# Performance work log

Hardware: AMD Instinct MI355X
Metric: run time of the kernel (lower is better)

The kernel has to match this reference:

```python
import jax, jax.numpy as jnp
import numpy as np

H = 50  # LSTM units, fixed in the original module


def setup_inputs() -> dict:
    key = jax.random.key(0)
    ks = jax.random.split(key, 5)
    B, T, F = 4096, 365, 32
    scale = 0.1
    return {
        "x": jax.random.normal(ks[0], (B, T, F), jnp.float32),
        "kernel": jax.random.normal(ks[1], (F, 4 * H), jnp.float32) * scale,
        "rec_kernel": jax.random.normal(ks[2], (H, 4 * H), jnp.float32) * scale,
        "bias": jax.random.normal(ks[3], (4 * H,), jnp.float32) * scale,
        "dense_w": jax.random.normal(ks[4], (H, 1), jnp.float32) * scale,
        "dense_b": jnp.zeros((1,), jnp.float32),
    }


def _lstm_last_h(x, kernel, rec_kernel, bias):
    # Keras LSTM, gate order [i, f, c, o]; activation=relu, recurrent_activation=sigmoid.
    B = x.shape[0]
    # Precompute input contribution for all timesteps: [B, T, 4H]
    xg = jnp.einsum("btf,fg->btg", x, kernel) + bias
    h0 = jnp.zeros((B, H), x.dtype)
    c0 = jnp.zeros((B, H), x.dtype)

    def step(carry, xt):  # xt: [B, 4H]
        h, c = carry
        g = xt + h @ rec_kernel
        i = jax.nn.sigmoid(g[:, :H])
        f = jax.nn.sigmoid(g[:, H:2 * H])
        cand = jax.nn.relu(g[:, 2 * H:3 * H])
        o = jax.nn.sigmoid(g[:, 3 * H:])
        c_new = f * c + i * cand
        h_new = o * jax.nn.relu(c_new)
        return (h_new, c_new), None

    (h_last, _), _ = jax.lax.scan(step, (h0, c0), jnp.swapaxes(xg, 0, 1))
    return h_last  # [B, H]


def reference(x, kernel, rec_kernel, bias, dense_w, dense_b):
    h = _lstm_last_h(x, kernel, rec_kernel, bias)
    return h @ dense_w + dense_b  # [B, 1]
```

## Files before the change

kernel.cpp:

```cpp
#include <hip/hip_runtime.h>


typedef _Float16 f16;
typedef f16 f16x4 __attribute__((ext_vector_type(4)));
typedef float f32x4 __attribute__((ext_vector_type(4)));

#define T_STEPS 365
#define F_IN    32
#define H_U     50
#define NG      200
#define AST     72
#define GST     212

__global__ __launch_bounds__(256)
void lstm_fused(const float* __restrict__ x,
                const float* __restrict__ wk,
                const float* __restrict__ wr,
                const float* __restrict__ bias,
                const float* __restrict__ dw,
                const float* __restrict__ db,
                float* __restrict__ out)
{
    __shared__ f16   As[2][16 * AST];
    __shared__ float Gs[16 * GST];

    const int tid  = threadIdx.x;
    const int lane = tid & 63;
    const int w    = tid >> 6;
    const int cl   = lane & 15;
    const int lg   = lane >> 4;
    const long row0 = (long)blockIdx.x * 16;

    int nj[4]; nj[0] = w; nj[1] = w + 4; nj[2] = w + 8; nj[3] = 12;

    f16x4 bf[4][6];
    #pragma unroll
    for (int j = 0; j < 4; ++j) {
        const int n = nj[j];
        const int u = 4 * n + (cl >> 2);
        const int g = cl & 3;
        const int corig = g * H_U + u;
        const bool cv = (u < H_U) && (j != 3 || w == 3);
        #pragma unroll
        for (int ks = 0; ks < 6; ++ks) {
            f16x4 v;
            #pragma unroll
            for (int e = 0; e < 4; ++e) {
                const int k = ks * 16 + lg * 4 + e;
                float wv = 0.f;
                if (cv) {
                    if (k < 32)      wv = wk[k * NG + corig];
                    else if (k < 82) wv = wr[(k - 32) * NG + corig];
                    else if (k == 82) wv = bias[corig];
                }
                v[e] = (f16)wv;
            }
            bf[j][ks] = v;
        }
    }

    for (int i = tid; i < 16 * AST; i += 256) { As[0][i] = (f16)0.f; As[1][i] = (f16)0.f; }
    __syncthreads();
    if (tid < 16) { As[0][tid * AST + 50] = (f16)1.f; As[1][tid * AST + 50] = (f16)1.f; }
    __syncthreads();

    const float* xrow = x + (row0 + cl) * (long)(T_STEPS * F_IN);
    float4 xlA = *(const float4*)(xrow + 0 * F_IN + 4 * lg);
    float4 xhA = *(const float4*)(xrow + 0 * F_IN + 4 * lg + 16);
    float4 xlB = *(const float4*)(xrow + 1 * F_IN + 4 * lg);
    float4 xhB = *(const float4*)(xrow + 1 * F_IN + 4 * lg + 16);

    float c0 = 0.f, c1 = 0.f, c2 = 0.f, c3 = 0.f;

    auto step = [&](int t, float4& xl, float4& xh) {
        const int p = t & 1;
        f16x4 a0, a1, ah[4];
        a0[0] = (f16)xl.x; a0[1] = (f16)xl.y; a0[2] = (f16)xl.z; a0[3] = (f16)xl.w;
        a1[0] = (f16)xh.x; a1[1] = (f16)xh.y; a1[2] = (f16)xh.z; a1[3] = (f16)xh.w;
        #pragma unroll
        for (int jp = 0; jp < 4; ++jp)
            ah[jp] = *(const f16x4*)&As[p][cl * AST + 16 * jp + 4 * lg];
        if (t + 2 < T_STEPS) {
            xl = *(const float4*)(xrow + (t + 2) * F_IN + 4 * lg);
            xh = *(const float4*)(xrow + (t + 2) * F_IN + 4 * lg + 16);
        }
        #pragma unroll
        for (int j = 0; j < 4; ++j) {
            if (j != 3 || w == 3) {
                const int n = nj[j];
                f32x4 acc = {0.f, 0.f, 0.f, 0.f};
                acc = __builtin_amdgcn_mfma_f32_16x16x16f16(a0,    bf[j][0], acc, 0, 0, 0);
                acc = __builtin_amdgcn_mfma_f32_16x16x16f16(a1,    bf[j][1], acc, 0, 0, 0);
                acc = __builtin_amdgcn_mfma_f32_16x16x16f16(ah[0], bf[j][2], acc, 0, 0, 0);
                acc = __builtin_amdgcn_mfma_f32_16x16x16f16(ah[1], bf[j][3], acc, 0, 0, 0);
                acc = __builtin_amdgcn_mfma_f32_16x16x16f16(ah[2], bf[j][4], acc, 0, 0, 0);
                acc = __builtin_amdgcn_mfma_f32_16x16x16f16(ah[3], bf[j][5], acc, 0, 0, 0);
                #pragma unroll
                for (int e = 0; e < 4; ++e)
                    Gs[(4 * lg + e) * GST + 16 * n + cl] = acc[e];
            }
        }
        #pragma unroll
        for (int j = 0; j < 4; ++j) {
            const bool valid = (j != 3) || (w == 3 && lg < 2);
            if (valid) {
                const int n = nj[j];
                const int u = 4 * n + lg;
                const f32x4 g4 = *(const f32x4*)&Gs[cl * GST + 16 * n + 4 * lg];
                const float ig = __builtin_amdgcn_rcpf(1.f + __expf(-g4[0]));
                const float fg = __builtin_amdgcn_rcpf(1.f + __expf(-g4[1]));
                const float cd = fmaxf(g4[2], 0.f);
                const float og = __builtin_amdgcn_rcpf(1.f + __expf(-g4[3]));
                float& c = (j == 0) ? c0 : ((j == 1) ? c1 : ((j == 2) ? c2 : c3));
                c = fg * c + ig * cd;
                const float hv = og * fmaxf(c, 0.f);
                As[p ^ 1][cl * AST + u] = (f16)hv;
            }
        }
        __syncthreads();
    };

    for (int m = 0; m < (T_STEPS - 1) / 2; ++m) {
        step(2 * m,     xlA, xhA);
        step(2 * m + 1, xlB, xhB);
    }
    step(T_STEPS - 1, xlA, xhA);

    if (tid < 16) {
        float acc = db[0];
        #pragma unroll
        for (int u = 0; u < H_U; ++u)
            acc += (float)As[1][tid * AST + u] * dw[u];
        out[row0 + tid] = acc;
    }
}

extern "C" void kernel_launch(void* const* d_in, const int* in_sizes, int n_in,
                              void* d_out, int out_size, void* d_ws, size_t ws_size,
                              hipStream_t stream) {
    (void)in_sizes; (void)n_in; (void)d_ws; (void)ws_size; (void)out_size;
    const float* x  = (const float*)d_in[0];
    const float* wk = (const float*)d_in[1];
    const float* wr = (const float*)d_in[2];
    const float* bs = (const float*)d_in[3];
    const float* dw = (const float*)d_in[4];
    const float* db = (const float*)d_in[5];
    float* out = (float*)d_out;
    hipLaunchKernelGGL(lstm_fused, dim3(4096 / 16), dim3(256), 0, stream,
                       x, wk, wr, bs, dw, db, out);
}
```

Before: 455.2 us.

## Swap MFMA operands to keep gates in registers and use 8 waves

The MFMA operands are swapped (weights as A, activations as B), so each lane's accumulator holds the four gates of one unit for one batch row. This removes the shared-memory gate staging buffer and its extra read-back pass. The block grows to 512 threads (8 waves), each wave owning one or two 16-column tiles, and the barrier becomes an inline s_waitcnt plus s_barrier. This trades fewer per-wave MFMAs for more waves contending at the per-step barrier.

```diff
diff --git a/kernel.cpp b/kernel.cpp
--- a/kernel.cpp
+++ b/kernel.cpp
@@ -10,9 +10,8 @@
 #define H_U     50
 #define NG      200
 #define AST     72
-#define GST     212
 
-__global__ __launch_bounds__(256)
+__global__ __launch_bounds__(512)
 void lstm_fused(const float* __restrict__ x,
                 const float* __restrict__ wk,
                 const float* __restrict__ wr,
@@ -21,8 +20,7 @@
                 const float* __restrict__ db,
                 float* __restrict__ out)
 {
-    __shared__ f16   As[2][16 * AST];
-    __shared__ float Gs[16 * GST];
+    __shared__ f16 As[2][16 * AST];
 
     const int tid  = threadIdx.x;
     const int lane = tid & 63;
@@ -31,35 +29,35 @@
     const int lg   = lane >> 4;
     const long row0 = (long)blockIdx.x * 16;
 
-    int nj[4]; nj[0] = w; nj[1] = w + 4; nj[2] = w + 8; nj[3] = 12;
+    const int n0 = w;
+    const int n1 = w + 8;
+    const bool has1 = (w < 5);
 
-    f16x4 bf[4][6];
-    #pragma unroll
-    for (int j = 0; j < 4; ++j) {
-        const int n = nj[j];
-        const int u = 4 * n + (cl >> 2);
-        const int g = cl & 3;
-        const int corig = g * H_U + u;
-        const bool cv = (u < H_U) && (j != 3 || w == 3);
+    f16x4 bf0[6], bf1[6];
+    {
+        const int u0 = 4 * n0 + (cl >> 2);
+        const int u1 = 4 * n1 + (cl >> 2);
+        const int g  = cl & 3;
+        const int c0 = g * H_U + u0;
+        const int c1 = g * H_U + u1;
+        const bool v1ok = has1 && (u1 < H_U);
         #pragma unroll
         for (int ks = 0; ks < 6; ++ks) {
-            f16x4 v;
+            f16x4 v0, v1;
             #pragma unroll
             for (int e = 0; e < 4; ++e) {
                 const int k = ks * 16 + lg * 4 + e;
-                float wv = 0.f;
-                if (cv) {
-                    if (k < 32)      wv = wk[k * NG + corig];
-                    else if (k < 82) wv = wr[(k - 32) * NG + corig];
-                    else if (k == 82) wv = bias[corig];
-                }
-                v[e] = (f16)wv;
+                float w0 = 0.f, w1 = 0.f;
+                if (k < 32)       { w0 = wk[k * NG + c0];        if (v1ok) w1 = wk[k * NG + c1]; }
+                else if (k < 82)  { w0 = wr[(k - 32) * NG + c0]; if (v1ok) w1 = wr[(k - 32) * NG + c1]; }
+                else if (k == 82) { w0 = bias[c0];               if (v1ok) w1 = bias[c1]; }
+                v0[e] = (f16)w0; v1[e] = (f16)w1;
             }
-            bf[j][ks] = v;
+            bf0[ks] = v0; bf1[ks] = v1;
         }
     }
 
-    for (int i = tid; i < 16 * AST; i += 256) { As[0][i] = (f16)0.f; As[1][i] = (f16)0.f; }
+    for (int i = tid; i < 16 * AST; i += 512) { As[0][i] = (f16)0.f; As[1][i] = (f16)0.f; }
     __syncthreads();
     if (tid < 16) { As[0][tid * AST + 50] = (f16)1.f; As[1][tid * AST + 50] = (f16)1.f; }
     __syncthreads();
@@ -70,54 +68,56 @@
     float4 xlB = *(const float4*)(xrow + 1 * F_IN + 4 * lg);
     float4 xhB = *(const float4*)(xrow + 1 * F_IN + 4 * lg + 16);
 
-    float c0 = 0.f, c1 = 0.f, c2 = 0.f, c3 = 0.f;
+    float c0 = 0.f, c1 = 0.f;
+    const int u_0 = 4 * n0 + lg;
+    const int u_1 = 4 * n1 + lg;
+    const bool wr1 = has1 && (u_1 < H_U);
 
     auto step = [&](int t, float4& xl, float4& xh) {
         const int p = t & 1;
         f16x4 a0, a1, ah[4];
-        a0[0] = (f16)xl.x; a0[1] = (f16)xl.y; a0[2] = (f16)xl.z; a0[3] = (f16)xl.w;
-        a1[0] = (f16)xh.x; a1[1] = (f16)xh.y; a1[2] = (f16)xh.z; a1[3] = (f16)xh.w;
         #pragma unroll
         for (int jp = 0; jp < 4; ++jp)
             ah[jp] = *(const f16x4*)&As[p][cl * AST + 16 * jp + 4 * lg];
+        a0[0] = (f16)xl.x; a0[1] = (f16)xl.y; a0[2] = (f16)xl.z; a0[3] = (f16)xl.w;
+        a1[0] = (f16)xh.x; a1[1] = (f16)xh.y; a1[2] = (f16)xh.z; a1[3] = (f16)xh.w;
         if (t + 2 < T_STEPS) {
             xl = *(const float4*)(xrow + (t + 2) * F_IN + 4 * lg);
             xh = *(const float4*)(xrow + (t + 2) * F_IN + 4 * lg + 16);
         }
-        #pragma unroll
-        for (int j = 0; j < 4; ++j) {
-            if (j != 3 || w == 3) {
-                const int n = nj[j];
-                f32x4 acc = {0.f, 0.f, 0.f, 0.f};
-                acc = __builtin_amdgcn_mfma_f32_16x16x16f16(a0,    bf[j][0], acc, 0, 0, 0);
-                acc = __builtin_amdgcn_mfma_f32_16x16x16f16(a1,    bf[j][1], acc, 0, 0, 0);
-                acc = __builtin_amdgcn_mfma_f32_16x16x16f16(ah[0], bf[j][2], acc, 0, 0, 0);
-                acc = __builtin_amdgcn_mfma_f32_16x16x16f16(ah[1], bf[j][3], acc, 0, 0, 0);
-                acc = __builtin_amdgcn_mfma_f32_16x16x16f16(ah[2], bf[j][4], acc, 0, 0, 0);
-                acc = __builtin_amdgcn_mfma_f32_16x16x16f16(ah[3], bf[j][5], acc, 0, 0, 0);
-                #pragma unroll
-                for (int e = 0; e < 4; ++e)
-                    Gs[(4 * lg + e) * GST + 16 * n + cl] = acc[e];
-            }
+        f32x4 acc0 = {0.f, 0.f, 0.f, 0.f};
+        acc0 = __builtin_amdgcn_mfma_f32_16x16x16f16(bf0[0], a0,    acc0, 0, 0, 0);
+        acc0 = __builtin_amdgcn_mfma_f32_16x16x16f16(bf0[1], a1,    acc0, 0, 0, 0);
+        acc0 = __builtin_amdgcn_mfma_f32_16x16x16f16(bf0[2], ah[0], acc0, 0, 0, 0);
+        acc0 = __builtin_amdgcn_mfma_f32_16x16x16f16(bf0[3], ah[1], acc0, 0, 0, 0);
+        acc0 = __builtin_amdgcn_mfma_f32_16x16x16f16(bf0[4], ah[2], acc0, 0, 0, 0);
+        acc0 = __builtin_amdgcn_mfma_f32_16x16x16f16(bf0[5], ah[3], acc0, 0, 0, 0);
+        f32x4 acc1 = {0.f, 0.f, 0.f, 0.f};
+        if (has1) {
+            acc1 = __builtin_amdgcn_mfma_f32_16x16x16f16(bf1[0], a0,    acc1, 0, 0, 0);
+            acc1 = __builtin_amdgcn_mfma_f32_16x16x16f16(bf1[1], a1,    acc1, 0, 0, 0);
+            acc1 = __builtin_amdgcn_mfma_f32_16x16x16f16(bf1[2], ah[0], acc1, 0, 0, 0);
+            acc1 = __builtin_amdgcn_mfma_f32_16x16x16f16(bf1[3], ah[1], acc1, 0, 0, 0);
+            acc1 = __builtin_amdgcn_mfma_f32_16x16x16f16(bf1[4], ah[2], acc1, 0, 0, 0);
+            acc1 = __builtin_amdgcn_mfma_f32_16x16x16f16(bf1[5], ah[3], acc1, 0, 0, 0);
         }
-        #pragma unroll
-        for (int j = 0; j < 4; ++j) {
-            const bool valid = (j != 3) || (w == 3 && lg < 2);
-            if (valid) {
-                const int n = nj[j];
-                const int u = 4 * n + lg;
-                const f32x4 g4 = *(const f32x4*)&Gs[cl * GST + 16 * n + 4 * lg];
-                const float ig = __builtin_amdgcn_rcpf(1.f + __expf(-g4[0]));
-                const float fg = __builtin_amdgcn_rcpf(1.f + __expf(-g4[1]));
-                const float cd = fmaxf(g4[2], 0.f);
-                const float og = __builtin_amdgcn_rcpf(1.f + __expf(-g4[3]));
-                float& c = (j == 0) ? c0 : ((j == 1) ? c1 : ((j == 2) ? c2 : c3));
-                c = fg * c + ig * cd;
-                const float hv = og * fmaxf(c, 0.f);
-                As[p ^ 1][cl * AST + u] = (f16)hv;
-            }
+        {
+            const float ig = __builtin_amdgcn_rcpf(1.f + __expf(-acc0[0]));
+            const float fg = __builtin_amdgcn_rcpf(1.f + __expf(-acc0[1]));
+            const float cd = fmaxf(acc0[2], 0.f);
+            const float og = __builtin_amdgcn_rcpf(1.f + __expf(-acc0[3]));
+            c0 = fg * c0 + ig * cd;
+            As[p ^ 1][cl * AST + u_0] = (f16)(og * fmaxf(c0, 0.f));
         }
-        __syncthreads();
+        if (wr1) {
+            const float ig = __builtin_amdgcn_rcpf(1.f + __expf(-acc1[0]));
+            const float fg = __builtin_amdgcn_rcpf(1.f + __expf(-acc1[1]));
+            const float cd = fmaxf(acc1[2], 0.f);
+            const float og = __builtin_amdgcn_rcpf(1.f + __expf(-acc1[3]));
+            c1 = fg * c1 + ig * cd;
+            As[p ^ 1][cl * AST + u_1] = (f16)(og * fmaxf(c1, 0.f));
+        }
+        asm volatile("s_waitcnt lgkmcnt(0)\n\ts_barrier" ::: "memory");
     };
 
     for (int m = 0; m < (T_STEPS - 1) / 2; ++m) {
@@ -146,6 +146,6 @@
     const float* dw = (const float*)d_in[4];
     const float* db = (const float*)d_in[5];
     float* out = (float*)d_out;
-    hipLaunchKernelGGL(lstm_fused, dim3(4096 / 16), dim3(256), 0, stream,
+    hipLaunchKernelGGL(lstm_fused, dim3(4096 / 16), dim3(512), 0, stream,
                        x, wk, wr, bs, dw, db, out);
 }
```

Measured after the change: 459.4 us. No clear change (+0.9%).
